# Performance work log

Hardware: AMD Instinct MI355X
Metric: run time of the kernel (lower is better)

## Reference

```python
import jax, jax.numpy as jnp
import numpy as np

PROCESSING_STEPS = 3


def setup_inputs() -> dict:
    key = jax.random.key(0)
    ks = jax.random.split(key, 6)
    N, D, G = 500000, 128, 4096
    x = jax.random.normal(ks[0], (N, D), dtype=jnp.float32)
    # torch LSTM param layout: [4*hidden, input] and [4*hidden, hidden], gates i,f,g,o
    s = 1.0 / np.sqrt(D)
    W_ih = jax.random.uniform(ks[1], (4 * D, 2 * D), minval=-s, maxval=s, dtype=jnp.float32)
    W_hh = jax.random.uniform(ks[2], (4 * D, D), minval=-s, maxval=s, dtype=jnp.float32)
    b_ih = jax.random.uniform(ks[3], (4 * D,), minval=-s, maxval=s, dtype=jnp.float32)
    b_hh = jax.random.uniform(ks[4], (4 * D,), minval=-s, maxval=s, dtype=jnp.float32)
    index = jnp.sort(jax.random.randint(ks[5], (N,), 0, G, dtype=jnp.int64))
    return {"x": x, "W_ih": W_ih, "W_hh": W_hh, "b_ih": b_ih, "b_hh": b_hh,
            "index": index, "dim_size": G}


def _lstm_cell(inp, h, c, W_ih, W_hh, b_ih, b_hh):
    gates = inp @ W_ih.T + h @ W_hh.T + (b_ih + b_hh)  # [G, 4D]
    i, f, g, o = jnp.split(gates, 4, axis=-1)
    c = jax.nn.sigmoid(f) * c + jax.nn.sigmoid(i) * jnp.tanh(g)
    h = jax.nn.sigmoid(o) * jnp.tanh(c)
    return h, c


def reference(x, W_ih, W_hh, b_ih, b_hh, index, dim_size):
    N, D = x.shape
    h = jnp.zeros((dim_size, D), dtype=x.dtype)
    c = jnp.zeros((dim_size, D), dtype=x.dtype)
    q_star = jnp.zeros((dim_size, 2 * D), dtype=x.dtype)
    for _ in range(PROCESSING_STEPS):
        h, c = _lstm_cell(q_star, h, c, W_ih, W_hh, b_ih, b_hh)
        q = h  # [G, D]
        e = jnp.sum(x * q[index], axis=-1)  # [N]
        # segment softmax (numerically stable)
        m = jax.ops.segment_max(e, index, num_segments=dim_size)
        m = jnp.where(jnp.isfinite(m), m, 0.0)  # guard empty segments
        ex = jnp.exp(e - m[index])
        s = jax.ops.segment_sum(ex, index, num_segments=dim_size)
        a = ex / jnp.maximum(s, 1e-16)[index]  # [N]
        r = jax.ops.segment_sum(a[:, None] * x, index, num_segments=dim_size)  # [G, D]
        q_star = jnp.concatenate([q, r], axis=-1)
    return q_star
```

## Files before the change

kernel.cpp:

```cpp
#include <hip/hip_runtime.h>
#include <hip/hip_fp16.h>
#include <math.h>

#define D 128

__device__ __forceinline__ float sigmoidf_(float x) { return 1.f / (1.f + __expf(-x)); }

__global__ void prep_kernel(const float* __restrict__ W_ih, const float* __restrict__ W_hh,
                            const float* __restrict__ b_ih, const float* __restrict__ b_hh,
                            const int* __restrict__ idx, int N, int G,
                            float* __restrict__ Wc, int* __restrict__ seg_off,
                            float* __restrict__ b_sum, float* __restrict__ h1,
                            float* __restrict__ c1) {
    int b = blockIdx.x, t = threadIdx.x;
    if (b < 256) {
        int i = b * 256 + t;
        int j = i >> 7, k = i & (D - 1);
        Wc[i] = W_ih[(size_t)j * (2 * D) + k] + W_hh[i];
    } else if (b < 273) {
        int g = (b - 256) * 256 + t;
        if (g <= G) {
            int lo = 0, hi = N;
            while (lo < hi) {
                int mid = (lo + hi) >> 1;
                if (idx[mid] < g) lo = mid + 1; else hi = mid;
            }
            seg_off[g] = lo;
        }
    } else {
        for (int i = t; i < 4 * D; i += 256) b_sum[i] = b_ih[i] + b_hh[i];
        if (t < D) {
            float bi = b_ih[t] + b_hh[t];
            float bg = b_ih[2 * D + t] + b_hh[2 * D + t];
            float bo = b_ih[3 * D + t] + b_hh[3 * D + t];
            float c = sigmoidf_(bi) * tanhf(bg);
            c1[t] = c;
            h1[t] = sigmoidf_(bo) * tanhf(c);
        }
    }
}

__global__ __launch_bounds__(256) void x_to_h_kernel(const float* __restrict__ x,
                                                     __half* __restrict__ xh,
                                                     size_t total) {
    size_t i = ((size_t)blockIdx.x * 256 + threadIdx.x) * 8;
    if (i >= total) return;
    float4 a = *(const float4*)&x[i];
    float4 b = *(const float4*)&x[i + 4];
    __half2 h[4];
    h[0] = __floats2half2_rn(a.x, a.y);
    h[1] = __floats2half2_rn(a.z, a.w);
    h[2] = __floats2half2_rn(b.x, b.y);
    h[3] = __floats2half2_rn(b.z, b.w);
    *(float4*)&xh[i] = *(float4*)h;
}

__global__ __launch_bounds__(256) void attn_kernel(
    const __half* __restrict__ xh, const int* __restrict__ seg_off,
    const float* __restrict__ q, int q_stride,
    float* __restrict__ r_out, int r_stride, int G) {
    int g = blockIdx.x;
    if (g >= G) return;
    int tid = threadIdx.x;
    int wave = tid >> 6, lane = tid & 63;
    int qg = lane >> 4;
    int c = lane & 15;

    __shared__ float sm[4], ss[4];
    __shared__ float sacc[4][D];

    int start = seg_off[g], end = seg_off[g + 1];
    int count = end - start;
    int chunk = (count + 3) >> 2;
    int wsr = start + wave * chunk;
    int wer = min(wsr + chunk, end);

    const float4* x4 = (const float4*)xh;
    const float* qrow = q + (size_t)g * q_stride;
    float4 q0 = *(const float4*)&qrow[8 * c];
    float4 q1 = *(const float4*)&qrow[8 * c + 4];

    float m = -INFINITY, s = 0.f;
    float acc[8] = {0.f, 0.f, 0.f, 0.f, 0.f, 0.f, 0.f, 0.f};

    if (wsr < wer) {
        int last = wer - 1;
        for (int base = wsr; base < wer; base += 8) {
            int r0 = min(base + qg, last);
            int r1 = min(base + 4 + qg, last);
            float4 v0 = x4[(size_t)r0 * 16 + c];
            float4 v1 = x4[(size_t)r1 * 16 + c];
            const __half2* h0 = (const __half2*)&v0;
            const __half2* h1 = (const __half2*)&v1;
            float2 a0 = __half22float2(h0[0]), a1 = __half22float2(h0[1]);
            float2 a2 = __half22float2(h0[2]), a3 = __half22float2(h0[3]);
            float2 b0 = __half22float2(h1[0]), b1 = __half22float2(h1[1]);
            float2 b2 = __half22float2(h1[2]), b3 = __half22float2(h1[3]);
            float xf0[8] = {a0.x, a0.y, a1.x, a1.y, a2.x, a2.y, a3.x, a3.y};
            float xf1[8] = {b0.x, b0.y, b1.x, b1.y, b2.x, b2.y, b3.x, b3.y};

            float p0 = xf0[0] * q0.x + xf0[1] * q0.y + xf0[2] * q0.z + xf0[3] * q0.w
                     + xf0[4] * q1.x + xf0[5] * q1.y + xf0[6] * q1.z + xf0[7] * q1.w;
            float p1 = xf1[0] * q0.x + xf1[1] * q0.y + xf1[2] * q0.z + xf1[3] * q0.w
                     + xf1[4] * q1.x + xf1[5] * q1.y + xf1[6] * q1.z + xf1[7] * q1.w;
#pragma unroll
            for (int off = 1; off < 16; off <<= 1) {
                p0 += __shfl_xor(p0, off);
                p1 += __shfl_xor(p1, off);
            }
            float p0a = __shfl_xor(p0, 16), p0b = __shfl_xor(p0, 32), p0c = __shfl_xor(p0a, 32);
            float p1a = __shfl_xor(p1, 16), p1b = __shfl_xor(p1, 32), p1c = __shfl_xor(p1a, 32);
            float s00 = (base + qg       < wer) ? p0  : -INFINITY;
            float s01 = (base + (qg ^ 1) < wer) ? p0a : -INFINITY;
            float s02 = (base + (qg ^ 2) < wer) ? p0b : -INFINITY;
            float s03 = (base + (qg ^ 3) < wer) ? p0c : -INFINITY;
            float s10 = (base + 4 + qg       < wer) ? p1  : -INFINITY;
            float s11 = (base + 4 + (qg ^ 1) < wer) ? p1a : -INFINITY;
            float s12 = (base + 4 + (qg ^ 2) < wer) ? p1b : -INFINITY;
            float s13 = (base + 4 + (qg ^ 3) < wer) ? p1c : -INFINITY;

            float mn = fmaxf(fmaxf(fmaxf(s00, s01), fmaxf(s02, s03)),
                             fmaxf(fmaxf(s10, s11), fmaxf(s12, s13)));
            mn = fmaxf(m, mn);
            float al = __expf(m - mn);
            float w00 = __expf(s00 - mn), w01 = __expf(s01 - mn);
            float w02 = __expf(s02 - mn), w03 = __expf(s03 - mn);
            float w10 = __expf(s10 - mn), w11 = __expf(s11 - mn);
            float w12 = __expf(s12 - mn), w13 = __expf(s13 - mn);
            float sg = (w00 + w01) + (w02 + w03) + ((w10 + w11) + (w12 + w13));
            s = s * al + sg;
#pragma unroll
            for (int j = 0; j < 8; ++j)
                acc[j] = acc[j] * al + w00 * xf0[j] + w10 * xf1[j];
            m = mn;
        }
    }
#pragma unroll
    for (int j = 0; j < 8; ++j) {
        acc[j] += __shfl_xor(acc[j], 16);
        acc[j] += __shfl_xor(acc[j], 32);
    }
    if (lane == 0) { sm[wave] = m; ss[wave] = s; }
    if (qg == 0) {
#pragma unroll
        for (int j = 0; j < 8; ++j) sacc[wave][8 * c + j] = acc[j];
    }
    __syncthreads();

    if (tid < D) {
        float m0 = sm[0], m1 = sm[1], m2 = sm[2], m3 = sm[3];
        float mstar = fmaxf(fmaxf(m0, m1), fmaxf(m2, m3));
        float r = 0.f;
        if (mstar > -INFINITY) {
            float e0 = __expf(m0 - mstar), e1 = __expf(m1 - mstar);
            float e2 = __expf(m2 - mstar), e3 = __expf(m3 - mstar);
            float stot = ss[0] * e0 + ss[1] * e1 + ss[2] * e2 + ss[3] * e3;
            float at = sacc[0][tid] * e0 + sacc[1][tid] * e1
                     + sacc[2][tid] * e2 + sacc[3][tid] * e3;
            r = at / fmaxf(stot, 1e-16f);
        }
        r_out[(size_t)g * r_stride + tid] = r;
    }
}

__global__ __launch_bounds__(256) void gates_gemm_kernel(
    const float* __restrict__ A1, int sA1,
    const float* __restrict__ W1,
    const float* __restrict__ A2,
    const float* __restrict__ W2, int sW2,
    const float* __restrict__ bias,
    float* __restrict__ gates) {
    __shared__ float As[32][72];
    __shared__ float Ws[32][72];
    int t = threadIdx.x;
    int tx = t & 15, ty = t >> 4;
    int g0 = blockIdx.x * 64, j0 = blockIdx.y * 64;
    int lr = t & 63;
    int lk = (t >> 6) * 8;

    float acc[4][4];
#pragma unroll
    for (int i = 0; i < 4; ++i)
#pragma unroll
        for (int j = 0; j < 4; ++j) acc[i][j] = 0.f;

    for (int phase = 0; phase < 2; ++phase) {
        const float* A = phase ? A2 : A1;
        int sA = phase ? D : sA1;
        const float* W = phase ? W2 : W1;
        int sW = phase ? sW2 : D;
        for (int kk = 0; kk < D; kk += 32) {
            float4 a0 = *(const float4*)&A[(size_t)(g0 + lr) * sA + kk + lk];
            float4 a1 = *(const float4*)&A[(size_t)(g0 + lr) * sA + kk + lk + 4];
            float4 w0 = *(const float4*)&W[(size_t)(j0 + lr) * sW + kk + lk];
            float4 w1 = *(const float4*)&W[(size_t)(j0 + lr) * sW + kk + lk + 4];
            __syncthreads();
            As[lk + 0][lr] = a0.x; As[lk + 1][lr] = a0.y; As[lk + 2][lr] = a0.z; As[lk + 3][lr] = a0.w;
            As[lk + 4][lr] = a1.x; As[lk + 5][lr] = a1.y; As[lk + 6][lr] = a1.z; As[lk + 7][lr] = a1.w;
            Ws[lk + 0][lr] = w0.x; Ws[lk + 1][lr] = w0.y; Ws[lk + 2][lr] = w0.z; Ws[lk + 3][lr] = w0.w;
            Ws[lk + 4][lr] = w1.x; Ws[lk + 5][lr] = w1.y; Ws[lk + 6][lr] = w1.z; Ws[lk + 7][lr] = w1.w;
            __syncthreads();
#pragma unroll
            for (int k = 0; k < 32; ++k) {
                float4 av = *(const float4*)&As[k][ty * 4];
                float4 bv = *(const float4*)&Ws[k][tx * 4];
                float aa[4] = {av.x, av.y, av.z, av.w};
                float bb[4] = {bv.x, bv.y, bv.z, bv.w};
#pragma unroll
                for (int i = 0; i < 4; ++i)
#pragma unroll
                    for (int j = 0; j < 4; ++j)
                        acc[i][j] = fmaf(aa[i], bb[j], acc[i][j]);
            }
        }
    }
#pragma unroll
    for (int i = 0; i < 4; ++i) {
        size_t row = (size_t)(g0 + ty * 4 + i);
        int jb = j0 + tx * 4;
        float4 o;
        o.x = acc[i][0] + bias[jb + 0];
        o.y = acc[i][1] + bias[jb + 1];
        o.z = acc[i][2] + bias[jb + 2];
        o.w = acc[i][3] + bias[jb + 3];
        *(float4*)&gates[row * 512 + jb] = o;
    }
}

__global__ void cell_kernel(const float* __restrict__ gates,
                            const float* __restrict__ c_prev, int c_stride,
                            float* __restrict__ c_out,
                            float* __restrict__ h_out, int h_stride,
                            int total) {
    int t = blockIdx.x * blockDim.x + threadIdx.x;
    if (t >= total) return;
    int g = t >> 7, k = t & (D - 1);
    const float* grow = gates + (size_t)g * 512;
    float ig = grow[k];
    float fg = grow[D + k];
    float gg = grow[2 * D + k];
    float og = grow[3 * D + k];
    float cp = c_prev[(size_t)g * c_stride + k];
    float c = sigmoidf_(fg) * cp + sigmoidf_(ig) * tanhf(gg);
    float h = sigmoidf_(og) * tanhf(c);
    c_out[t] = c;
    h_out[(size_t)g * h_stride + k] = h;
}

extern "C" void kernel_launch(void* const* d_in, const int* in_sizes, int n_in,
                              void* d_out, int out_size, void* d_ws, size_t ws_size,
                              hipStream_t stream) {
    const float* x      = (const float*)d_in[0];
    const float* W_ih   = (const float*)d_in[1];
    const float* W_hh   = (const float*)d_in[2];
    const float* b_ih   = (const float*)d_in[3];
    const float* b_hh   = (const float*)d_in[4];
    const int*   index  = (const int*)d_in[5];
    int N = in_sizes[5];
    int G = out_size / (2 * D);
    float* out = (float*)d_out;
    size_t totalx = (size_t)N * D;

    float* ws = (float*)d_ws;
    __half* xh    = (__half*)ws;
    float* Wc     = ws + totalx / 2;
    float* b_sum  = Wc + 4 * D * D;
    float* h1     = b_sum + 4 * D;
    float* c1     = h1 + D;
    float* r1     = c1 + D;
    float* h2     = r1 + (size_t)G * D;
    float* c2     = h2 + (size_t)G * D;
    float* r2     = c2 + (size_t)G * D;
    float* gatesb = r2 + (size_t)G * D;
    int* seg_off  = (int*)(gatesb + (size_t)G * 4 * D);
    float* c3     = r1;

    prep_kernel<<<274, 256, 0, stream>>>(W_ih, W_hh, b_ih, b_hh, index, N, G,
                                         Wc, seg_off, b_sum, h1, c1);
    x_to_h_kernel<<<(int)((totalx / 8 + 255) / 256), 256, 0, stream>>>(x, xh, totalx);

    attn_kernel<<<G, 256, 0, stream>>>(xh, seg_off, h1, 0, r1, D, G);

    gates_gemm_kernel<<<dim3(G / 64, 8), 256, 0, stream>>>(
        h1, 0, Wc, r1, W_ih + D, 2 * D, b_sum, gatesb);
    cell_kernel<<<(G * D + 255) / 256, 256, 0, stream>>>(gatesb, c1, 0, c2, h2, D, G * D);
    attn_kernel<<<G, 256, 0, stream>>>(xh, seg_off, h2, D, r2, D, G);

    gates_gemm_kernel<<<dim3(G / 64, 8), 256, 0, stream>>>(
        h2, D, Wc, r2, W_ih + D, 2 * D, b_sum, gatesb);
    cell_kernel<<<(G * D + 255) / 256, 256, 0, stream>>>(gatesb, c2, D, c3, out, 2 * D, G * D);
    attn_kernel<<<G, 256, 0, stream>>>(xh, seg_off, out, 2 * D, out + D, 2 * D, G);
}
```

Baseline: 493.6 us.

## Fuse fp16 conversion into first attention pass and LSTM cell into attention

The standalone x-to-half conversion kernel is removed. The first attention pass now reads fp32 x directly, computes with it and writes the fp16 copy as it goes, which saves one full read of x. The LSTM cell elementwise kernel is folded into the start of the later attention kernels: each block computes h and c for its segment and stages h in shared memory as the query. This removes two launches and a round trip of h through global memory, at the cost of a block-wide barrier before the attention loop and heavier per-row traffic in the first pass.

Measured after the change: 481.3 us. 1.03x faster.

```diff
diff --git a/kernel.cpp b/kernel.cpp
--- a/kernel.cpp
+++ b/kernel.cpp
@@ -5,6 +5,15 @@
 #define D 128
 
 __device__ __forceinline__ float sigmoidf_(float x) { return 1.f / (1.f + __expf(-x)); }
+
+__device__ __forceinline__ float4 pack8_to_half8(const float* xf) {
+    __half2 hh[4];
+    hh[0] = __floats2half2_rn(xf[0], xf[1]);
+    hh[1] = __floats2half2_rn(xf[2], xf[3]);
+    hh[2] = __floats2half2_rn(xf[4], xf[5]);
+    hh[3] = __floats2half2_rn(xf[6], xf[7]);
+    return *(float4*)hh;
+}
 
 __global__ void prep_kernel(const float* __restrict__ W_ih, const float* __restrict__ W_hh,
                             const float* __restrict__ b_ih, const float* __restrict__ b_hh,
@@ -40,24 +49,119 @@
     }
 }
 
-__global__ __launch_bounds__(256) void x_to_h_kernel(const float* __restrict__ x,
-                                                     __half* __restrict__ xh,
-                                                     size_t total) {
-    size_t i = ((size_t)blockIdx.x * 256 + threadIdx.x) * 8;
-    if (i >= total) return;
-    float4 a = *(const float4*)&x[i];
-    float4 b = *(const float4*)&x[i + 4];
-    __half2 h[4];
-    h[0] = __floats2half2_rn(a.x, a.y);
-    h[1] = __floats2half2_rn(a.z, a.w);
-    h[2] = __floats2half2_rn(b.x, b.y);
-    h[3] = __floats2half2_rn(b.z, b.w);
-    *(float4*)&xh[i] = *(float4*)h;
-}
-
-__global__ __launch_bounds__(256) void attn_kernel(
+__global__ __launch_bounds__(256) void attn_first_kernel(
+    const float* __restrict__ x, __half* __restrict__ xh,
+    const int* __restrict__ seg_off, const float* __restrict__ q,
+    float* __restrict__ r_out, int G) {
+    int g = blockIdx.x;
+    if (g >= G) return;
+    int tid = threadIdx.x;
+    int wave = tid >> 6, lane = tid & 63;
+    int qg = lane >> 4;
+    int c = lane & 15;
+
+    __shared__ float sm[4], ss[4];
+    __shared__ float sacc[4][D];
+
+    int start = seg_off[g], end = seg_off[g + 1];
+    int count = end - start;
+    int chunk = (count + 3) >> 2;
+    int wsr = start + wave * chunk;
+    int wer = min(wsr + chunk, end);
+
+    const float4* x4 = (const float4*)x;
+    float4* xh4 = (float4*)xh;
+    float4 q0 = *(const float4*)&q[8 * c];
+    float4 q1 = *(const float4*)&q[8 * c + 4];
+
+    float m = -INFINITY, s = 0.f;
+    float acc[8] = {0.f, 0.f, 0.f, 0.f, 0.f, 0.f, 0.f, 0.f};
+
+    if (wsr < wer) {
+        int last = wer - 1;
+        for (int base = wsr; base < wer; base += 8) {
+            int r0 = min(base + qg, last);
+            int r1 = min(base + 4 + qg, last);
+            float4 f00 = x4[(size_t)r0 * 32 + 2 * c];
+            float4 f01 = x4[(size_t)r0 * 32 + 2 * c + 1];
+            float4 f10 = x4[(size_t)r1 * 32 + 2 * c];
+            float4 f11 = x4[(size_t)r1 * 32 + 2 * c + 1];
+            float xf0[8] = {f00.x, f00.y, f00.z, f00.w, f01.x, f01.y, f01.z, f01.w};
+            float xf1[8] = {f10.x, f10.y, f10.z, f10.w, f11.x, f11.y, f11.z, f11.w};
+
+            xh4[(size_t)r0 * 16 + c] = pack8_to_half8(xf0);
+            xh4[(size_t)r1 * 16 + c] = pack8_to_half8(xf1);
+
+            float p0 = xf0[0] * q0.x + xf0[1] * q0.y + xf0[2] * q0.z + xf0[3] * q0.w
+                     + xf0[4] * q1.x + xf0[5] * q1.y + xf0[6] * q1.z + xf0[7] * q1.w;
+            float p1 = xf1[0] * q0.x + xf1[1] * q0.y + xf1[2] * q0.z + xf1[3] * q0.w
+                     + xf1[4] * q1.x + xf1[5] * q1.y + xf1[6] * q1.z + xf1[7] * q1.w;
+#pragma unroll
+            for (int off = 1; off < 16; off <<= 1) {
+                p0 += __shfl_xor(p0, off);
+                p1 += __shfl_xor(p1, off);
+            }
+            float p0a = __shfl_xor(p0, 16), p0b = __shfl_xor(p0, 32), p0c = __shfl_xor(p0a, 32);
+            float p1a = __shfl_xor(p1, 16), p1b = __shfl_xor(p1, 32), p1c = __shfl_xor(p1a, 32);
+            float s00 = (base + qg       < wer) ? p0  : -INFINITY;
+            float s01 = (base + (qg ^ 1) < wer) ? p0a : -INFINITY;
+            float s02 = (base + (qg ^ 2) < wer) ? p0b : -INFINITY;
+            float s03 = (base + (qg ^ 3) < wer) ? p0c : -INFINITY;
+            float s10 = (base + 4 + qg       < wer) ? p1  : -INFINITY;
+            float s11 = (base + 4 + (qg ^ 1) < wer) ? p1a : -INFINITY;
+            float s12 = (base + 4 + (qg ^ 2) < wer) ? p1b : -INFINITY;
+            float s13 = (base + 4 + (qg ^ 3) < wer) ? p1c : -INFINITY;
+
+            float mn = fmaxf(fmaxf(fmaxf(s00, s01), fmaxf(s02, s03)),
+                             fmaxf(fmaxf(s10, s11), fmaxf(s12, s13)));
+            mn = fmaxf(m, mn);
+            float al = __expf(m - mn);
+            float w00 = __expf(s00 - mn), w01 = __expf(s01 - mn);
+            float w02 = __expf(s02 - mn), w03 = __expf(s03 - mn);
+            float w10 = __expf(s10 - mn), w11 = __expf(s11 - mn);
+            float w12 = __expf(s12 - mn), w13 = __expf(s13 - mn);
+            float sg = (w00 + w01) + (w02 + w03) + ((w10 + w11) + (w12 + w13));
+            s = s * al + sg;
+#pragma unroll
+            for (int j = 0; j < 8; ++j)
+                acc[j] = acc[j] * al + w00 * xf0[j] + w10 * xf1[j];
+            m = mn;
+        }
+    }
+#pragma unroll
+    for (int j = 0; j < 8; ++j) {
+        acc[j] += __shfl_xor(acc[j], 16);
+        acc[j] += __shfl_xor(acc[j], 32);
+    }
+    if (lane == 0) { sm[wave] = m; ss[wave] = s; }
+    if (qg == 0) {
+#pragma unroll
+        for (int j = 0; j < 8; ++j) sacc[wave][8 * c + j] = acc[j];
+    }
+    __syncthreads();
+
+    if (tid < D) {
+        float m0 = sm[0], m1 = sm[1], m2 = sm[2], m3 = sm[3];
+        float mstar = fmaxf(fmaxf(m0, m1), fmaxf(m2, m3));
+        float r = 0.f;
+        if (mstar > -INFINITY) {
+            float e0 = __expf(m0 - mstar), e1 = __expf(m1 - mstar);
+            float e2 = __expf(m2 - mstar), e3 = __expf(m3 - mstar);
+            float stot = ss[0] * e0 + ss[1] * e1 + ss[2] * e2 + ss[3] * e3;
+            float at = sacc[0][tid] * e0 + sacc[1][tid] * e1
+                     + sacc[2][tid] * e2 + sacc[3][tid] * e3;
+            r = at / fmaxf(stot, 1e-16f);
+        }
+        r_out[(size_t)g * D + tid] = r;
+    }
+}
+
+__global__ __launch_bounds__(256) void attn_cell_kernel(
     const __half* __restrict__ xh, const int* __restrict__ seg_off,
-    const float* __restrict__ q, int q_stride,
+    const float* __restrict__ gates,
+    const float* __restrict__ c_prev, int c_stride,
+    float* __restrict__ c_out,
+    float* __restrict__ h_out, int h_stride,
     float* __restrict__ r_out, int r_stride, int G) {
     int g = blockIdx.x;
     if (g >= G) return;
@@ -68,6 +172,22 @@
 
     __shared__ float sm[4], ss[4];
     __shared__ float sacc[4][D];
+    __shared__ float qsh[D];
+
+    if (tid < D) {
+        const float* grow = gates + (size_t)g * 512;
+        float ig = grow[tid];
+        float fg = grow[D + tid];
+        float gg = grow[2 * D + tid];
+        float og = grow[3 * D + tid];
+        float cp = c_prev[(size_t)g * c_stride + tid];
+        float cc = sigmoidf_(fg) * cp + sigmoidf_(ig) * tanhf(gg);
+        float hh = sigmoidf_(og) * tanhf(cc);
+        if (c_out) c_out[(size_t)g * D + tid] = cc;
+        h_out[(size_t)g * h_stride + tid] = hh;
+        qsh[tid] = hh;
+    }
+    __syncthreads();
 
     int start = seg_off[g], end = seg_off[g + 1];
     int count = end - start;
@@ -76,9 +196,8 @@
     int wer = min(wsr + chunk, end);
 
     const float4* x4 = (const float4*)xh;
-    const float* qrow = q + (size_t)g * q_stride;
-    float4 q0 = *(const float4*)&qrow[8 * c];
-    float4 q1 = *(const float4*)&qrow[8 * c + 4];
+    float4 q0 = *(const float4*)&qsh[8 * c];
+    float4 q1 = *(const float4*)&qsh[8 * c + 4];
 
     float m = -INFINITY, s = 0.f;
     float acc[8] = {0.f, 0.f, 0.f, 0.f, 0.f, 0.f, 0.f, 0.f};
@@ -227,26 +346,6 @@
     }
 }
 
-__global__ void cell_kernel(const float* __restrict__ gates,
-                            const float* __restrict__ c_prev, int c_stride,
-                            float* __restrict__ c_out,
-                            float* __restrict__ h_out, int h_stride,
-                            int total) {
-    int t = blockIdx.x * blockDim.x + threadIdx.x;
-    if (t >= total) return;
-    int g = t >> 7, k = t & (D - 1);
-    const float* grow = gates + (size_t)g * 512;
-    float ig = grow[k];
-    float fg = grow[D + k];
-    float gg = grow[2 * D + k];
-    float og = grow[3 * D + k];
-    float cp = c_prev[(size_t)g * c_stride + k];
-    float c = sigmoidf_(fg) * cp + sigmoidf_(ig) * tanhf(gg);
-    float h = sigmoidf_(og) * tanhf(c);
-    c_out[t] = c;
-    h_out[(size_t)g * h_stride + k] = h;
-}
-
 extern "C" void kernel_launch(void* const* d_in, const int* in_sizes, int n_in,
                               void* d_out, int out_size, void* d_ws, size_t ws_size,
                               hipStream_t stream) {
@@ -273,21 +372,19 @@
     float* r2     = c2 + (size_t)G * D;
     float* gatesb = r2 + (size_t)G * D;
     int* seg_off  = (int*)(gatesb + (size_t)G * 4 * D);
-    float* c3     = r1;
 
     prep_kernel<<<274, 256, 0, stream>>>(W_ih, W_hh, b_ih, b_hh, index, N, G,
                                          Wc, seg_off, b_sum, h1, c1);
-    x_to_h_kernel<<<(int)((totalx / 8 + 255) / 256), 256, 0, stream>>>(x, xh, totalx);
-
-    attn_kernel<<<G, 256, 0, stream>>>(xh, seg_off, h1, 0, r1, D, G);
+
+    attn_first_kernel<<<G, 256, 0, stream>>>(x, xh, seg_off, h1, r1, G);
 
     gates_gemm_kernel<<<dim3(G / 64, 8), 256, 0, stream>>>(
         h1, 0, Wc, r1, W_ih + D, 2 * D, b_sum, gatesb);
-    cell_kernel<<<(G * D + 255) / 256, 256, 0, stream>>>(gatesb, c1, 0, c2, h2, D, G * D);
-    attn_kernel<<<G, 256, 0, stream>>>(xh, seg_off, h2, D, r2, D, G);
+    attn_cell_kernel<<<G, 256, 0, stream>>>(
+        xh, seg_off, gatesb, c1, 0, c2, h2, D, r2, D, G);
 
     gates_gemm_kernel<<<dim3(G / 64, 8), 256, 0, stream>>>(
         h2, D, Wc, r2, W_ih + D, 2 * D, b_sum, gatesb);
-    cell_kernel<<<(G * D + 255) / 256, 256, 0, stream>>>(gatesb, c2, D, c3, out, 2 * D, G * D);
-    attn_kernel<<<G, 256, 0, stream>>>(xh, seg_off, out, 2 * D, out + D, 2 * D, G);
-}
+    attn_cell_kernel<<<G, 256, 0, stream>>>(
+        xh, seg_off, gatesb, c2, D, nullptr, out, 2 * D, out + D, 2 * D, G);
+}
```
